# Kernel optimization log

Hardware: AMD Instinct MI355X
Metric: run time of the kernel (lower is better)

The kernel has to match this reference:

```python
import jax, jax.numpy as jnp
import numpy as np

SEQ, B, IN, H, L = 2048, 64, 512, 512, 2

def _xavier(key, shape):
    fan_out, fan_in = shape
    bound = float(np.sqrt(6.0 / (fan_in + fan_out)))
    return jax.random.uniform(key, shape, jnp.float32, -bound, bound)

def setup_inputs() -> dict:
    key = jax.random.key(0)
    ks = jax.random.split(key, 5)
    x = jax.random.normal(ks[0], (SEQ, B, IN), jnp.float32)
    # layer 0: input_size=IN; layer 1: input_size=H. Biases init to zeros (reset_parameters).
    return {
        "x": x,
        "W_ih0": _xavier(ks[1], (H, IN)),
        "W_hh0": _xavier(ks[2], (H, H)),
        "b_ih0": jnp.zeros((H,), jnp.float32),
        "b_hh0": jnp.zeros((H,), jnp.float32),
        "W_ih1": _xavier(ks[3], (H, H)),
        "W_hh1": _xavier(ks[4], (H, H)),
        "b_ih1": jnp.zeros((H,), jnp.float32),
        "b_hh1": jnp.zeros((H,), jnp.float32),
    }

def _run_layer(x_in, W_ih, W_hh, b_ih, b_hh):
    # Precompute input projection for all timesteps (matches forward_optimized / same math as forward).
    proj = jnp.einsum('sbi,hi->sbh', x_in, W_ih) + b_ih  # [S,B,H]
    h0 = jnp.zeros((x_in.shape[1], W_hh.shape[0]), x_in.dtype)
    def step(h, p_t):
        h_new = jnp.tanh(p_t + h @ W_hh.T + b_hh)
        return h_new, h_new
    h_final, outs = jax.lax.scan(step, h0, proj)
    return outs, h_final

def reference(x, W_ih0, W_hh0, b_ih0, b_hh0, W_ih1, W_hh1, b_ih1, b_hh1):
    out0, h0 = _run_layer(x, W_ih0, W_hh0, b_ih0, b_hh0)
    out1, h1 = _run_layer(out0, W_ih1, W_hh1, b_ih1, b_hh1)
    hidden = jnp.stack([h0, h1], axis=0)  # [num_layers, B, H]
    return out1, hidden
```

## Files before the change

### kernel.cpp

```cpp
#include <hip/hip_runtime.h>
#include <cstdint>
#include <cstddef>

#define SEQ   2048
#define BATCH 64
#define HID   512

__global__ __launch_bounds__(256)
void proj_gemm(const float* __restrict__ A, const float* __restrict__ W,
               const float* __restrict__ bias, float* __restrict__ C)
{
    __shared__ float As[16][132];
    __shared__ float Bs[16][132];
    const int t  = threadIdx.x;
    const int bm = blockIdx.x >> 2;
    const int bn = blockIdx.x & 3;
    const int m0 = bm * 128;
    const int n0 = bn * 128;
    const int tn = t & 15;
    const int tm = t >> 4;

    float acc[8][8];
#pragma unroll
    for (int i = 0; i < 8; ++i)
#pragma unroll
        for (int j = 0; j < 8; ++j) acc[i][j] = 0.f;

    const int lrow = t >> 2;
    const int lk4  = t & 3;

    for (int kk = 0; kk < 512; kk += 16) {
#pragma unroll
        for (int i = 0; i < 2; ++i) {
            const int row = lrow + i * 64;
            float4 va = *(const float4*)&A[(size_t)(m0 + row) * 512 + kk + lk4 * 4];
            As[lk4 * 4 + 0][row] = va.x;
            As[lk4 * 4 + 1][row] = va.y;
            As[lk4 * 4 + 2][row] = va.z;
            As[lk4 * 4 + 3][row] = va.w;
            float4 vb = *(const float4*)&W[(size_t)(n0 + row) * 512 + kk + lk4 * 4];
            Bs[lk4 * 4 + 0][row] = vb.x;
            Bs[lk4 * 4 + 1][row] = vb.y;
            Bs[lk4 * 4 + 2][row] = vb.z;
            Bs[lk4 * 4 + 3][row] = vb.w;
        }
        __syncthreads();
#pragma unroll
        for (int k = 0; k < 16; ++k) {
            float4 a0 = *(const float4*)&As[k][tm * 8];
            float4 a1 = *(const float4*)&As[k][tm * 8 + 4];
            float4 b0 = *(const float4*)&Bs[k][tn * 4];
            float4 b1 = *(const float4*)&Bs[k][64 + tn * 4];
            float ar[8] = {a0.x, a0.y, a0.z, a0.w, a1.x, a1.y, a1.z, a1.w};
            float bc[8] = {b0.x, b0.y, b0.z, b0.w, b1.x, b1.y, b1.z, b1.w};
#pragma unroll
            for (int i = 0; i < 8; ++i)
#pragma unroll
                for (int j = 0; j < 8; ++j)
                    acc[i][j] = fmaf(ar[i], bc[j], acc[i][j]);
        }
        __syncthreads();
    }

    float4 bv0 = *(const float4*)&bias[n0 + tn * 4];
    float4 bv1 = *(const float4*)&bias[n0 + 64 + tn * 4];
    const float bb[8] = {bv0.x, bv0.y, bv0.z, bv0.w, bv1.x, bv1.y, bv1.z, bv1.w};
#pragma unroll
    for (int i = 0; i < 8; ++i) {
        const size_t rowoff = (size_t)(m0 + tm * 8 + i) * 512 + n0;
        float4 o0, o1;
        o0.x = acc[i][0] + bb[0]; o0.y = acc[i][1] + bb[1];
        o0.z = acc[i][2] + bb[2]; o0.w = acc[i][3] + bb[3];
        o1.x = acc[i][4] + bb[4]; o1.y = acc[i][5] + bb[5];
        o1.z = acc[i][6] + bb[6]; o1.w = acc[i][7] + bb[7];
        *(float4*)&C[rowoff + tn * 4] = o0;
        *(float4*)&C[rowoff + 64 + tn * 4] = o1;
    }
}

__global__ __launch_bounds__(512, 2)
void rnn_scan(const float* __restrict__ proj, const float* __restrict__ Whh,
              const float* __restrict__ bhh, float* __restrict__ out,
              float* __restrict__ hidden, unsigned long long* __restrict__ hbuf)
{
    __shared__ float hS[2][528];

    const int t   = threadIdx.x;
    const int bid = blockIdx.x;
    const int s   = bid >> 6;
    const int b   = bid & 63;
    const int w   = t >> 6;
    const int l   = t & 63;
    const int lr  = l & 15;
    const int lc  = l >> 4;
    const int row = s * 128 + w * 16 + lr;

    float Wr[128];
    {
        const float* wsrc = &Whh[(size_t)row * HID + lc * 128];
#pragma unroll
        for (int j = 0; j < 32; ++j) {
            float4 v = *(const float4*)&wsrc[j * 4];
            Wr[j * 4 + 0] = v.x; Wr[j * 4 + 1] = v.y;
            Wr[j * 4 + 2] = v.z; Wr[j * 4 + 3] = v.w;
        }
#pragma unroll
        for (int j = 0; j < 128; ++j) asm volatile("" : "+v"(Wr[j]));
    }
    const float breg = bhh[row];

    for (int i = t; i < 528; i += 512) { hS[0][i] = 0.f; hS[1][i] = 0.f; }
    __syncthreads();

    const bool own   = (t >> 7) == s;
    const int  pad_t = t + ((t >> 7) << 2);

    for (int step = 0; step < SEQ; ++step) {
        const int p = step & 1;

        float pv = 0.f;
        size_t oidx = 0;
        if (lc == 0) {
            oidx = ((size_t)step * BATCH + b) * HID + row;
            pv = proj[oidx];
        }

        if (!own) {
            const unsigned long long* src =
                hbuf + (size_t)p * (BATCH * HID) + (size_t)b * HID + t;
            const unsigned int want = (unsigned int)step;
            unsigned long long x;
            int spins = 0;
            for (;;) {
                x = __hip_atomic_load(src, __ATOMIC_RELAXED, __HIP_MEMORY_SCOPE_AGENT);
                if ((unsigned int)(x >> 32) == want) break;
                __builtin_amdgcn_s_sleep(1);
                if (++spins > 8192) {
                    __builtin_amdgcn_fence(__ATOMIC_ACQUIRE, "agent");
                    spins = 0;
                }
            }
            hS[p][pad_t] = __uint_as_float((unsigned int)x);
        }
        __syncthreads();

        const float* hp = &hS[p][lc * 132];
        float a0 = 0.f, a1 = 0.f, a2 = 0.f, a3 = 0.f;
#pragma unroll
        for (int j = 0; j < 32; j += 4) {
            float4 h0 = *(const float4*)&hp[(j + 0) * 4];
            float4 h1 = *(const float4*)&hp[(j + 1) * 4];
            float4 h2 = *(const float4*)&hp[(j + 2) * 4];
            float4 h3 = *(const float4*)&hp[(j + 3) * 4];
            a0 = fmaf(Wr[j*4+ 0], h0.x, a0); a0 = fmaf(Wr[j*4+ 1], h0.y, a0);
            a0 = fmaf(Wr[j*4+ 2], h0.z, a0); a0 = fmaf(Wr[j*4+ 3], h0.w, a0);
            a1 = fmaf(Wr[j*4+ 4], h1.x, a1); a1 = fmaf(Wr[j*4+ 5], h1.y, a1);
            a1 = fmaf(Wr[j*4+ 6], h1.z, a1); a1 = fmaf(Wr[j*4+ 7], h1.w, a1);
            a2 = fmaf(Wr[j*4+ 8], h2.x, a2); a2 = fmaf(Wr[j*4+ 9], h2.y, a2);
            a2 = fmaf(Wr[j*4+10], h2.z, a2); a2 = fmaf(Wr[j*4+11], h2.w, a2);
            a3 = fmaf(Wr[j*4+12], h3.x, a3); a3 = fmaf(Wr[j*4+13], h3.y, a3);
            a3 = fmaf(Wr[j*4+14], h3.z, a3); a3 = fmaf(Wr[j*4+15], h3.w, a3);
        }
        float sum = (a0 + a1) + (a2 + a3);
        sum += __shfl_xor(sum, 16, 64);
        sum += __shfl_xor(sum, 32, 64);

        if (lc == 0) {
            const float hn = tanhf(pv + breg + sum);
            out[oidx] = hn;
            const unsigned long long pk =
                ((unsigned long long)(unsigned int)(step + 1) << 32) |
                (unsigned long long)__float_as_uint(hn);
            __hip_atomic_store(
                &hbuf[(size_t)(p ^ 1) * (BATCH * HID) + (size_t)b * HID + row],
                pk, __ATOMIC_RELAXED, __HIP_MEMORY_SCOPE_AGENT);
            hS[p ^ 1][row + ((row >> 7) << 2)] = hn;
            if (step == SEQ - 1) hidden[(size_t)b * HID + row] = hn;
        }
    }
}

extern "C" void kernel_launch(void* const* d_in, const int* in_sizes, int n_in,
                              void* d_out, int out_size, void* d_ws, size_t ws_size,
                              hipStream_t stream)
{
    (void)in_sizes; (void)n_in; (void)out_size; (void)ws_size;

    const float* x    = (const float*)d_in[0];
    const float* Wih0 = (const float*)d_in[1];
    const float* Whh0 = (const float*)d_in[2];
    const float* bih0 = (const float*)d_in[3];
    const float* bhh0 = (const float*)d_in[4];
    const float* Wih1 = (const float*)d_in[5];
    const float* Whh1 = (const float*)d_in[6];
    const float* bih1 = (const float*)d_in[7];
    const float* bhh1 = (const float*)d_in[8];

    float* out1   = (float*)d_out;
    float* hidden = out1 + (size_t)SEQ * BATCH * HID;

    float* proj = (float*)d_ws;
    unsigned long long* hbufA =
        (unsigned long long*)(proj + (size_t)SEQ * BATCH * HID);
    unsigned long long* hbufB = hbufA + (size_t)2 * BATCH * HID;

    hipMemsetAsync(hbufA, 0, (size_t)4 * BATCH * HID * sizeof(unsigned long long),
                   stream);

    proj_gemm<<<dim3(4096), dim3(256), 0, stream>>>(x, Wih0, bih0, proj);
    {
        const float* p = proj; const float* w = Whh0; const float* bb = bhh0;
        float* o = out1; float* hd = hidden; unsigned long long* hb = hbufA;
        void* args[] = {&p, &w, &bb, &o, &hd, &hb};
        hipLaunchCooperativeKernel((const void*)rnn_scan, dim3(256), dim3(512),
                                   args, 0, stream);
    }

    proj_gemm<<<dim3(4096), dim3(256), 0, stream>>>(out1, Wih1, bih1, proj);
    {
        const float* p = proj; const float* w = Whh1; const float* bb = bhh1;
        float* o = out1; float* hd = hidden + BATCH * HID; unsigned long long* hb = hbufB;
        void* args[] = {&p, &w, &bb, &o, &hd, &hb};
        hipLaunchCooperativeKernel((const void*)rnn_scan, dim3(256), dim3(512),
                                   args, 0, stream);
    }
}
```

Baseline: 7.999 ms.

## Prefetch next-step projection, drop spin sleep, use fast tanh in RNN scan

Reworks the recurrent scan step: the next timestep's projection value is loaded one iteration ahead, so its global-load latency sits off the critical path. The sleep in the flag-polling loop is removed and the fence interval shortened to cut wake-up latency. The libm tanhf is replaced with an exp2/rcp approximation, and the weight registers are restructured into float4 variables pinned each iteration. The fast tanh may lose accuracy for large inputs, and busy polling without sleep adds memory traffic.

```diff
diff --git a/kernel.cpp b/kernel.cpp
--- a/kernel.cpp
+++ b/kernel.cpp
@@ -78,6 +78,18 @@
     }
 }
 
+__device__ __forceinline__ float fast_tanh(float x)
+{
+    const float e = __builtin_amdgcn_exp2f(x * 2.88539008177793f);
+    return fmaf(-2.0f, __builtin_amdgcn_rcpf(e + 1.0f), 1.0f);
+}
+
+#define W_LOAD(i) float4 w##i = *(const float4*)&wsrc[(i) * 4]
+#define W_KEEP(i) asm volatile("" : "+v"(w##i.x), "+v"(w##i.y), "+v"(w##i.z), "+v"(w##i.w))
+#define FMA_BLK(i, acc) do { float4 hh = hq[i]; \
+    acc = fmaf(w##i.x, hh.x, acc); acc = fmaf(w##i.y, hh.y, acc); \
+    acc = fmaf(w##i.z, hh.z, acc); acc = fmaf(w##i.w, hh.w, acc); } while (0)
+
 __global__ __launch_bounds__(512, 2)
 void rnn_scan(const float* __restrict__ proj, const float* __restrict__ Whh,
               const float* __restrict__ bhh, float* __restrict__ out,
@@ -95,18 +107,16 @@
     const int lc  = l >> 4;
     const int row = s * 128 + w * 16 + lr;
 
-    float Wr[128];
-    {
-        const float* wsrc = &Whh[(size_t)row * HID + lc * 128];
-#pragma unroll
-        for (int j = 0; j < 32; ++j) {
-            float4 v = *(const float4*)&wsrc[j * 4];
-            Wr[j * 4 + 0] = v.x; Wr[j * 4 + 1] = v.y;
-            Wr[j * 4 + 2] = v.z; Wr[j * 4 + 3] = v.w;
-        }
-#pragma unroll
-        for (int j = 0; j < 128; ++j) asm volatile("" : "+v"(Wr[j]));
-    }
+    const float* wsrc = &Whh[(size_t)row * HID + lc * 128];
+    W_LOAD(0);  W_LOAD(1);  W_LOAD(2);  W_LOAD(3);
+    W_LOAD(4);  W_LOAD(5);  W_LOAD(6);  W_LOAD(7);
+    W_LOAD(8);  W_LOAD(9);  W_LOAD(10); W_LOAD(11);
+    W_LOAD(12); W_LOAD(13); W_LOAD(14); W_LOAD(15);
+    W_LOAD(16); W_LOAD(17); W_LOAD(18); W_LOAD(19);
+    W_LOAD(20); W_LOAD(21); W_LOAD(22); W_LOAD(23);
+    W_LOAD(24); W_LOAD(25); W_LOAD(26); W_LOAD(27);
+    W_LOAD(28); W_LOAD(29); W_LOAD(30); W_LOAD(31);
+
     const float breg = bhh[row];
 
     for (int i = t; i < 528; i += 512) { hS[0][i] = 0.f; hS[1][i] = 0.f; }
@@ -115,15 +125,25 @@
     const bool own   = (t >> 7) == s;
     const int  pad_t = t + ((t >> 7) << 2);
 
+    const bool pub = (lc == 0);
+    float pv_next = 0.f;
+    if (pub) pv_next = proj[(size_t)b * HID + row];
+
     for (int step = 0; step < SEQ; ++step) {
         const int p = step & 1;
 
-        float pv = 0.f;
-        size_t oidx = 0;
-        if (lc == 0) {
-            oidx = ((size_t)step * BATCH + b) * HID + row;
-            pv = proj[oidx];
-        }
+        const float pv = pv_next;
+        if (pub && step + 1 < SEQ)
+            pv_next = proj[((size_t)(step + 1) * BATCH + b) * HID + row];
+
+        W_KEEP(0);  W_KEEP(1);  W_KEEP(2);  W_KEEP(3);
+        W_KEEP(4);  W_KEEP(5);  W_KEEP(6);  W_KEEP(7);
+        W_KEEP(8);  W_KEEP(9);  W_KEEP(10); W_KEEP(11);
+        W_KEEP(12); W_KEEP(13); W_KEEP(14); W_KEEP(15);
+        W_KEEP(16); W_KEEP(17); W_KEEP(18); W_KEEP(19);
+        W_KEEP(20); W_KEEP(21); W_KEEP(22); W_KEEP(23);
+        W_KEEP(24); W_KEEP(25); W_KEEP(26); W_KEEP(27);
+        W_KEEP(28); W_KEEP(29); W_KEEP(30); W_KEEP(31);
 
         if (!own) {
             const unsigned long long* src =
@@ -134,8 +154,7 @@
             for (;;) {
                 x = __hip_atomic_load(src, __ATOMIC_RELAXED, __HIP_MEMORY_SCOPE_AGENT);
                 if ((unsigned int)(x >> 32) == want) break;
-                __builtin_amdgcn_s_sleep(1);
-                if (++spins > 8192) {
+                if (++spins > 1024) {
                     __builtin_amdgcn_fence(__ATOMIC_ACQUIRE, "agent");
                     spins = 0;
                 }
@@ -144,30 +163,23 @@
         }
         __syncthreads();
 
-        const float* hp = &hS[p][lc * 132];
+        const float4* hq = (const float4*)&hS[p][lc * 132];
         float a0 = 0.f, a1 = 0.f, a2 = 0.f, a3 = 0.f;
-#pragma unroll
-        for (int j = 0; j < 32; j += 4) {
-            float4 h0 = *(const float4*)&hp[(j + 0) * 4];
-            float4 h1 = *(const float4*)&hp[(j + 1) * 4];
-            float4 h2 = *(const float4*)&hp[(j + 2) * 4];
-            float4 h3 = *(const float4*)&hp[(j + 3) * 4];
-            a0 = fmaf(Wr[j*4+ 0], h0.x, a0); a0 = fmaf(Wr[j*4+ 1], h0.y, a0);
-            a0 = fmaf(Wr[j*4+ 2], h0.z, a0); a0 = fmaf(Wr[j*4+ 3], h0.w, a0);
-            a1 = fmaf(Wr[j*4+ 4], h1.x, a1); a1 = fmaf(Wr[j*4+ 5], h1.y, a1);
-            a1 = fmaf(Wr[j*4+ 6], h1.z, a1); a1 = fmaf(Wr[j*4+ 7], h1.w, a1);
-            a2 = fmaf(Wr[j*4+ 8], h2.x, a2); a2 = fmaf(Wr[j*4+ 9], h2.y, a2);
-            a2 = fmaf(Wr[j*4+10], h2.z, a2); a2 = fmaf(Wr[j*4+11], h2.w, a2);
-            a3 = fmaf(Wr[j*4+12], h3.x, a3); a3 = fmaf(Wr[j*4+13], h3.y, a3);
-            a3 = fmaf(Wr[j*4+14], h3.z, a3); a3 = fmaf(Wr[j*4+15], h3.w, a3);
-        }
+        FMA_BLK(0,  a0); FMA_BLK(1,  a1); FMA_BLK(2,  a2); FMA_BLK(3,  a3);
+        FMA_BLK(4,  a0); FMA_BLK(5,  a1); FMA_BLK(6,  a2); FMA_BLK(7,  a3);
+        FMA_BLK(8,  a0); FMA_BLK(9,  a1); FMA_BLK(10, a2); FMA_BLK(11, a3);
+        FMA_BLK(12, a0); FMA_BLK(13, a1); FMA_BLK(14, a2); FMA_BLK(15, a3);
+        FMA_BLK(16, a0); FMA_BLK(17, a1); FMA_BLK(18, a2); FMA_BLK(19, a3);
+        FMA_BLK(20, a0); FMA_BLK(21, a1); FMA_BLK(22, a2); FMA_BLK(23, a3);
+        FMA_BLK(24, a0); FMA_BLK(25, a1); FMA_BLK(26, a2); FMA_BLK(27, a3);
+        FMA_BLK(28, a0); FMA_BLK(29, a1); FMA_BLK(30, a2); FMA_BLK(31, a3);
         float sum = (a0 + a1) + (a2 + a3);
         sum += __shfl_xor(sum, 16, 64);
         sum += __shfl_xor(sum, 32, 64);
 
-        if (lc == 0) {
-            const float hn = tanhf(pv + breg + sum);
-            out[oidx] = hn;
+        if (pub) {
+            const float hn = fast_tanh(pv + breg + sum);
+            out[((size_t)step * BATCH + b) * HID + row] = hn;
             const unsigned long long pk =
                 ((unsigned long long)(unsigned int)(step + 1) << 32) |
                 (unsigned long long)__float_as_uint(hn);
```

After: 8.626 ms. 1.08x slower.
